# Performance work log

Measured on AMD Instinct MI355X. Metric: run time of the kernel, lower is better.

## Reference

```python
import jax, jax.numpy as jnp
import numpy as np

N_ATOMS = 25000
N_PAIRS = 500000
N_PROP = 16
C = 64          # channel width of pp/pi/ii/out layers
N_BASIS = 4     # radial basis functions per pair
DEPTH = 4       # number of GC blocks


def setup_inputs() -> dict:
    key = jax.random.key(0)
    ks = jax.random.split(key, 16)

    def w(k, shape):
        fan_in = shape[-2]
        return jax.random.normal(k, shape, jnp.float32) / jnp.sqrt(jnp.float32(fan_in))

    return {
        "ind_2": jax.random.randint(ks[0], (N_PAIRS, 2), 0, N_ATOMS),
        "prop": jax.random.normal(ks[1], (N_ATOMS, N_PROP), jnp.float32),
        "basis": jax.random.uniform(ks[2], (N_PAIRS, N_BASIS), jnp.float32),
        "pp0_w1": w(ks[3], (N_PROP, C)),
        "pp0_b1": jnp.zeros((C,), jnp.float32),
        "pp_w1": w(ks[4], (DEPTH - 1, C, C)),
        "pp_b1": jnp.zeros((DEPTH - 1, C), jnp.float32),
        "pp_w2": w(ks[5], (DEPTH, C, C)),
        "pp_b2": jnp.zeros((DEPTH, C), jnp.float32),
        "pi_w1": w(ks[6], (DEPTH, 2 * C, C)),
        "pi_b1": jnp.zeros((DEPTH, C), jnp.float32),
        "pi_w2": w(ks[7], (DEPTH, C, C * N_BASIS)),
        "pi_b2": jnp.zeros((DEPTH, C * N_BASIS), jnp.float32),
        "ii_w1": w(ks[8], (DEPTH, C, C)),
        "ii_w2": w(ks[9], (DEPTH, C, C)),
        "res0_w": w(ks[10], (N_PROP, C)),
        "out_w1": w(ks[11], (DEPTH, C, C)),
        "out_b1": jnp.zeros((DEPTH, C), jnp.float32),
        "out_w2": w(ks[12], (DEPTH, C, C)),
        "out_b2": jnp.zeros((DEPTH, C), jnp.float32),
        "out_wo": w(ks[13], (DEPTH, C, 1)),
    }


def _pinet_forward(ind_2, prop, basis,
                   pp0_w1, pp0_b1, pp_w1, pp_b1, pp_w2, pp_b2,
                   pi_w1, pi_b1, pi_w2, pi_b2,
                   ii_w1, ii_w2, res0_w,
                   out_w1, out_b1, out_w2, out_b2, out_wo):
    act = jnp.tanh
    n_atoms = prop.shape[0]
    n_basis = basis.shape[-1]
    c = pi_w2.shape[-1] // n_basis  # pi output channels
    depth = pp_w2.shape[0]
    ind_i = ind_2[:, 0]
    ind_j = ind_2[:, 1]

    p = prop
    output = jnp.zeros((n_atoms, out_wo.shape[-1]), p.dtype)
    for d in range(depth):
        # PPLayer (FFLayer with bias)
        if d == 0:
            h = act(p @ pp0_w1 + pp0_b1)
        else:
            h = act(p @ pp_w1[d - 1] + pp_b1[d - 1])
        h = act(h @ pp_w2[d] + pp_b2[d])
        # PILayer: gather pair endpoints, concat, FFLayer, basis contraction
        pij = jnp.concatenate([h[ind_i], h[ind_j]], axis=-1)  # (P, 2C)
        ww = act(pij @ pi_w1[d] + pi_b1[d])                   # (P, C)
        ww = act(ww @ pi_w2[d] + pi_b2[d])                    # (P, C*B)
        ww = ww.reshape(-1, c, n_basis)                       # (P, C, B)
        inter = jnp.einsum('pcb,pb->pc', ww, basis)           # (P, C)
        # IILayer (FFLayer, no bias)
        inter = act(inter @ ii_w1[d])
        inter = act(inter @ ii_w2[d])
        # IPLayer: scatter-sum pairs back to atoms
        newp = jax.ops.segment_sum(inter, ind_i, num_segments=n_atoms)
        # ResUpdate: linear projection if dims differ (block 0), else plain sum
        p = (p @ res0_w + newp) if d == 0 else (p + newp)
        # OutLayer: FFLayer + biasless linear, accumulated over depth
        o = act(p @ out_w1[d] + out_b1[d])
        o = act(o @ out_w2[d] + out_b2[d])
        output = output + o @ out_wo[d]
    return output


def reference(ind_2, prop, basis,
              pp0_w1, pp0_b1, pp_w1, pp_b1, pp_w2, pp_b2,
              pi_w1, pi_b1, pi_w2, pi_b2,
              ii_w1, ii_w2, res0_w,
              out_w1, out_b1, out_w2, out_b2, out_wo):
    return _pinet_forward(ind_2, prop, basis,
                          pp0_w1, pp0_b1, pp_w1, pp_b1, pp_w2, pp_b2,
                          pi_w1, pi_b1, pi_w2, pi_b2,
                          ii_w1, ii_w2, res0_w,
                          out_w1, out_b1, out_w2, out_b2, out_wo)
```

## Files before the change

kernel.cpp:

```cpp
#include <hip/hip_runtime.h>
#include <hip/hip_bf16.h>

#define N_ATOMS 25000
#define N_PAIRS 500000
#define DEPTH 4

typedef _Float16 f16x8 __attribute__((ext_vector_type(8)));
typedef float f32x16 __attribute__((ext_vector_type(16)));
typedef unsigned short u16;

__device__ __forceinline__ float tanh_fast(float x) {
    float e = __expf(2.0f * x);
    return 1.0f - 2.0f * __builtin_amdgcn_rcpf(e + 1.0f);
}

__device__ __forceinline__ void split_h(float x, u16& hi, u16& lo) {
    _Float16 h = (_Float16)x;
    _Float16 l = (_Float16)(x - (float)h);
    hi = *(u16*)&h;
    lo = *(u16*)&l;
}

__global__ __launch_bounds__(256)
void prep_kernel(const float* __restrict__ piW1, const float* __restrict__ piW2,
                 const float* __restrict__ iiW1, const float* __restrict__ iiW2,
                 u16* __restrict__ img1, u16* __restrict__ img2, u16* __restrict__ imgab) {
    int gid = blockIdx.x * 256 + threadIdx.x;
    int d = gid >> 15, e = gid & 32767;
    u16 hi, lo;
    if (e < 8192) {
        int k = e >> 6, n = e & 63;
        split_h(piW1[d * 8192 + e], hi, lo);
        int ntw = n >> 5, colb = n & 31;
        int ks = k >> 4, lh = (k >> 3) & 1, j = k & 7;
        int off = ((ntw * 8 + ks) * 64 + lh * 32 + colb) * 8 + j;
        img1[d * 16384 + 0 * 8192 + off] = hi;
        img1[d * 16384 + 1 * 8192 + off] = lo;
    } else if (e < 24576) {
        int s = e - 8192;
        int k = s >> 8, n = s & 255;
        split_h(piW2[d * 16384 + s], hi, lo);
        int ch = n >> 2, t = n & 3;
        int ntw = ch >> 5, colb = ch & 31;
        int ks = k >> 4, lh = (k >> 3) & 1, j = k & 7;
        int off = (((ntw * 4 + t) * 4 + ks) * 64 + lh * 32 + colb) * 8 + j;
        img2[d * 32768 + 0 * 16384 + off] = hi;
        img2[d * 32768 + 1 * 16384 + off] = lo;
    } else {
        int stage = (e < 28672) ? 0 : 1;
        int s = e - (stage ? 28672 : 24576);
        int k = s >> 6, n = s & 63;
        float x = stage ? iiW2[d * 4096 + s] : iiW1[d * 4096 + s];
        split_h(x, hi, lo);
        int ntw = n >> 5, colb = n & 31;
        int ks = k >> 4, lh = (k >> 3) & 1, j = k & 7;
        int off = ((ntw * 4 + ks) * 64 + lh * 32 + colb) * 8 + j;
        imgab[d * 16384 + (stage * 2 + 0) * 4096 + off] = hi;
        imgab[d * 16384 + (stage * 2 + 1) * 4096 + off] = lo;
    }
}

__global__ __launch_bounds__(256)
void prep_b2(const float* __restrict__ piB2, float* __restrict__ b2p) {
    int d = blockIdx.x, n = threadIdx.x;
    int ch = n >> 2, t = n & 3;
    int np = (ch >> 5) * 128 + t * 32 + (ch & 31);
    b2p[d * 256 + np] = piB2[d * 256 + n];
}

template <int K, bool IS_D0>
__global__ __launch_bounds__(256)
void atom_mlp(const float* __restrict__ p_in,
              const float* __restrict__ W1, const float* __restrict__ b1,
              const float* __restrict__ W2, const float* __restrict__ b2,
              const float* __restrict__ res0_w,
              _Float16* __restrict__ h_hi, _Float16* __restrict__ h_lo,
              float* __restrict__ acc_out) {
    __shared__ float sP[4][64];
    __shared__ float sH[4][64];
    int tid = threadIdx.x;
    int al = tid >> 6, c = tid & 63;
    int a = blockIdx.x * 4 + al;
    if (c < K) sP[al][c] = p_in[a * K + c];
    __syncthreads();
    float s = b1[c];
#pragma unroll
    for (int k = 0; k < K; ++k) s += sP[al][k] * W1[k * 64 + c];
    float t1 = tanh_fast(s);
    float r;
    if (IS_D0) {
        r = 0.f;
#pragma unroll
        for (int k = 0; k < 16; ++k) r += sP[al][k] * res0_w[k * 64 + c];
    } else {
        r = sP[al][c];
    }
    acc_out[a * 64 + c] = r;
    sH[al][c] = t1;
    __syncthreads();
    float s2 = b2[c];
#pragma unroll
    for (int k = 0; k < 64; ++k) s2 += sH[al][k] * W2[k * 64 + c];
    float hv = tanh_fast(s2);
    _Float16 hb = (_Float16)hv;
    h_hi[a * 64 + c] = hb;
    h_lo[a * 64 + c] = (_Float16)(hv - (float)hb);
}

__global__ __launch_bounds__(256)
void out_kernel(const float* __restrict__ p,
                const float* __restrict__ W1, const float* __restrict__ b1,
                const float* __restrict__ W2, const float* __restrict__ b2,
                const float* __restrict__ wo,
                float* __restrict__ out, int store) {
    __shared__ float sP[4][64];
    __shared__ float sH[4][64];
    int tid = threadIdx.x;
    int al = tid >> 6, c = tid & 63;
    int a = blockIdx.x * 4 + al;
    sP[al][c] = p[a * 64 + c];
    __syncthreads();
    float s = b1[c];
#pragma unroll
    for (int k = 0; k < 64; ++k) s += sP[al][k] * W1[k * 64 + c];
    sH[al][c] = tanh_fast(s);
    __syncthreads();
    float s2 = b2[c];
#pragma unroll
    for (int k = 0; k < 64; ++k) s2 += sH[al][k] * W2[k * 64 + c];
    float v = tanh_fast(s2) * wo[c];
#pragma unroll
    for (int off = 32; off > 0; off >>= 1) v += __shfl_down(v, off, 64);
    if (c == 0) {
        if (store) out[a] = v;
        else out[a] += v;
    }
}

#define MFMA __builtin_amdgcn_mfma_f32_32x32x16_f16

__global__ __launch_bounds__(512, 2)
void pair_kernel(const _Float16* __restrict__ hhi,
                 const _Float16* __restrict__ hlo,
                 const int* __restrict__ ind2,
                 const float* __restrict__ basis,
                 const u16* __restrict__ img1,
                 const u16* __restrict__ img2,
                 const u16* __restrict__ imgab,
                 const float* __restrict__ piB1,
                 const float* __restrict__ b2p,
                 float* __restrict__ accp) {
    __shared__ __attribute__((aligned(16))) _Float16 sW2[32768];
    __shared__ __attribute__((aligned(16))) _Float16 sW1lo[8192];
    __shared__ __attribute__((aligned(16))) _Float16 sA[16384];
    __shared__ __attribute__((aligned(16))) _Float16 sAlo[8192];
    __shared__ __attribute__((aligned(16))) _Float16 sPing[8192];
    __shared__ float sBas[128 * 4];
    __shared__ int sIdx[128];

    const int tid = threadIdx.x;
    for (int i = tid; i < 4096; i += 512) ((uint4*)sW2)[i] = ((const uint4*)img2)[i];
    for (int i = tid; i < 1024; i += 512) ((uint4*)sW1lo)[i] = ((const uint4*)(img1 + 8192))[i];

    const int l = tid & 63;
    const int w = tid >> 6;
    const int mt = w >> 1, ntw = w & 1;
    const int col = l & 31, kg = l >> 5;
    const int ch = ntw * 32 + col;
    const int chks = ch >> 4, chlh = (ch >> 3) & 1, chj = ch & 7;

    f16x8 w1h[8], fa[2][4], fb[2][4];
#pragma unroll
    for (int ks = 0; ks < 8; ++ks)
        w1h[ks] = *(const f16x8*)(img1 + ntw * 4096 + ks * 512 + l * 8);
#pragma unroll
    for (int hl = 0; hl < 2; ++hl)
#pragma unroll
        for (int ks = 0; ks < 4; ++ks) {
            fa[hl][ks] = *(const f16x8*)(imgab + (0 * 2 + hl) * 4096 + ntw * 2048 + ks * 512 + l * 8);
            fb[hl][ks] = *(const f16x8*)(imgab + (1 * 2 + hl) * 4096 + ntw * 2048 + ks * 512 + l * 8);
        }
    const float b1v = piB1[ch];
    float b2v[4];
#pragma unroll
    for (int t = 0; t < 4; ++t) b2v[t] = b2p[ntw * 128 + t * 32 + col];

    const int nTiles = (N_PAIRS + 127) >> 7;

    auto gather = [&](int tile) {
        int base = tile << 7;
#pragma unroll
        for (int it = 0; it < 6; ++it) {
            int id = it * 512 + tid;
            if (id < 2048) {
                int m = id >> 4, half = (id >> 3) & 1, seg = id & 7;
                int p = base + m;
                uint4 v = make_uint4(0u, 0u, 0u, 0u);
                if (p < N_PAIRS) {
                    int row = ind2[2 * p + half];
                    v = *(const uint4*)(hhi + row * 64 + seg * 8);
                }
                int mtd = m >> 5, lrow = m & 31;
                int ks = half * 4 + (seg >> 1), lh = seg & 1;
                *(uint4*)(sA + ((mtd * 8 + ks) * 64 + lh * 32 + lrow) * 8) = v;
            } else {
                int e = id - 2048;
                int m = e >> 3, seg = e & 7;
                int p = base + m;
                uint4 v = make_uint4(0u, 0u, 0u, 0u);
                if (p < N_PAIRS) {
                    int row = ind2[2 * p];
                    v = *(const uint4*)(hlo + row * 64 + seg * 8);
                }
                int mtd = m >> 5, lrow = m & 31;
                int ks = seg >> 1, lh = seg & 1;
                *(uint4*)(sAlo + ((mtd * 4 + ks) * 64 + lh * 32 + lrow) * 8) = v;
            }
        }
    };
    gather(blockIdx.x);
    __syncthreads();

    for (int tile = blockIdx.x; tile < nTiles; tile += gridDim.x) {
        const int base = tile << 7;

        if (tid < 128) {
            int p = base + tid;
            float4 bv = (p < N_PAIRS) ? ((const float4*)basis)[p] : make_float4(0.f, 0.f, 0.f, 0.f);
            *(float4*)&sBas[tid * 4] = bv;
            sIdx[tid] = (p < N_PAIRS) ? ind2[2 * p] : 0;
        }
        {
            f32x16 acc = {};
            const _Float16* ap = sA + mt * 4096 + l * 8;
            const _Float16* alop = sAlo + mt * 2048 + l * 8;
            const _Float16* blo = sW1lo + ntw * 4096 + l * 8;
#pragma unroll
            for (int ks = 0; ks < 8; ++ks) {
                f16x8 a = *(const f16x8*)(ap + ks * 512);
                acc = MFMA(a, w1h[ks], acc, 0, 0, 0);
                acc = MFMA(a, *(const f16x8*)(blo + ks * 512), acc, 0, 0, 0);
            }
#pragma unroll
            for (int ks = 0; ks < 4; ++ks) {
                f16x8 a = *(const f16x8*)(alop + ks * 512);
                acc = MFMA(a, w1h[ks], acc, 0, 0, 0);
            }
#pragma unroll
            for (int r = 0; r < 16; ++r) {
                int lrow = (r & 3) + 8 * (r >> 2) + 4 * kg;
                sPing[((mt * 4 + chks) * 64 + chlh * 32 + lrow) * 8 + chj] =
                    (_Float16)tanh_fast(acc[r] + b1v);
            }
        }
        __syncthreads();

        {
            f32x16 acc[4] = {{}, {}, {}, {}};
            const _Float16* ap = sPing + mt * 2048 + l * 8;
#pragma unroll
            for (int ks = 0; ks < 4; ++ks) {
                f16x8 a = *(const f16x8*)(ap + ks * 512);
#pragma unroll
                for (int t = 0; t < 4; ++t) {
                    acc[t] = MFMA(a, *(const f16x8*)(sW2 + ((ntw * 4 + t) * 4 + ks) * 512 + l * 8), acc[t], 0, 0, 0);
                    acc[t] = MFMA(a, *(const f16x8*)(sW2 + 16384 + ((ntw * 4 + t) * 4 + ks) * 512 + l * 8), acc[t], 0, 0, 0);
                }
            }
#pragma unroll
            for (int r = 0; r < 16; ++r) {
                int lrow = (r & 3) + 8 * (r >> 2) + 4 * kg;
                int row = mt * 32 + lrow;
                float4 bas = *(const float4*)&sBas[row * 4];
                float s = tanh_fast(acc[0][r] + b2v[0]) * bas.x
                        + tanh_fast(acc[1][r] + b2v[1]) * bas.y
                        + tanh_fast(acc[2][r] + b2v[2]) * bas.z
                        + tanh_fast(acc[3][r] + b2v[3]) * bas.w;
                sA[((mt * 4 + chks) * 64 + chlh * 32 + lrow) * 8 + chj] = (_Float16)s;
            }
        }
        __syncthreads();

        {
            f32x16 acc = {};
            const _Float16* ap = sA + mt * 2048 + l * 8;
#pragma unroll
            for (int ks = 0; ks < 4; ++ks) {
                f16x8 a = *(const f16x8*)(ap + ks * 512);
                acc = MFMA(a, fa[0][ks], acc, 0, 0, 0);
                acc = MFMA(a, fa[1][ks], acc, 0, 0, 0);
            }
#pragma unroll
            for (int r = 0; r < 16; ++r) {
                int lrow = (r & 3) + 8 * (r >> 2) + 4 * kg;
                sPing[((mt * 4 + chks) * 64 + chlh * 32 + lrow) * 8 + chj] =
                    (_Float16)tanh_fast(acc[r]);
            }
        }
        __syncthreads();

        {
            f16x8 afr[4];
            const _Float16* ap = sPing + mt * 2048 + l * 8;
#pragma unroll
            for (int ks = 0; ks < 4; ++ks) afr[ks] = *(const f16x8*)(ap + ks * 512);
            int idxr[16];
#pragma unroll
            for (int r = 0; r < 16; ++r)
                idxr[r] = sIdx[mt * 32 + (r & 3) + 8 * (r >> 2) + 4 * kg];

            gather(tile + gridDim.x);

            f32x16 acc = {};
#pragma unroll
            for (int ks = 0; ks < 4; ++ks) {
                acc = MFMA(afr[ks], fb[0][ks], acc, 0, 0, 0);
                acc = MFMA(afr[ks], fb[1][ks], acc, 0, 0, 0);
            }
#pragma unroll
            for (int r = 0; r < 16; ++r) {
                int lrow = (r & 3) + 8 * (r >> 2) + 4 * kg;
                int p = base + mt * 32 + lrow;
                if (p < N_PAIRS)
                    atomicAdd(&accp[idxr[r] * 64 + ch], tanh_fast(acc[r]));
            }
        }
        __syncthreads();
    }
}

extern "C" void kernel_launch(void* const* d_in, const int* in_sizes, int n_in,
                              void* d_out, int out_size, void* d_ws, size_t ws_size,
                              hipStream_t stream) {
    const int* ind2 = (const int*)d_in[0];
    const float* prop = (const float*)d_in[1];
    const float* basis = (const float*)d_in[2];
    const float* pp0_w1 = (const float*)d_in[3];
    const float* pp0_b1 = (const float*)d_in[4];
    const float* pp_w1 = (const float*)d_in[5];
    const float* pp_b1 = (const float*)d_in[6];
    const float* pp_w2 = (const float*)d_in[7];
    const float* pp_b2 = (const float*)d_in[8];
    const float* pi_w1 = (const float*)d_in[9];
    const float* pi_b1 = (const float*)d_in[10];
    const float* pi_w2 = (const float*)d_in[11];
    const float* pi_b2 = (const float*)d_in[12];
    const float* ii_w1 = (const float*)d_in[13];
    const float* ii_w2 = (const float*)d_in[14];
    const float* res0_w = (const float*)d_in[15];
    const float* out_w1 = (const float*)d_in[16];
    const float* out_b1 = (const float*)d_in[17];
    const float* out_w2 = (const float*)d_in[18];
    const float* out_b2 = (const float*)d_in[19];
    const float* out_wo = (const float*)d_in[20];
    float* out = (float*)d_out;

    float* B0 = (float*)d_ws;
    float* B1 = B0 + N_ATOMS * 64;
    _Float16* Hhi = (_Float16*)(B1 + N_ATOMS * 64);
    _Float16* Hlo = Hhi + N_ATOMS * 64;
    u16* img1 = (u16*)(Hlo + N_ATOMS * 64);
    u16* img2 = img1 + 4 * 16384;
    u16* imgab = img2 + 4 * 32768;
    float* b2p = (float*)(imgab + 4 * 16384);
    float* pbuf[2] = {B0, B1};

    prep_kernel<<<512, 256, 0, stream>>>(pi_w1, pi_w2, ii_w1, ii_w2, img1, img2, imgab);
    prep_b2<<<4, 256, 0, stream>>>(pi_b2, b2p);

    for (int d = 0; d < DEPTH; ++d) {
        float* acc = pbuf[d & 1];
        if (d == 0) {
            atom_mlp<16, true><<<N_ATOMS / 4, 256, 0, stream>>>(
                prop, pp0_w1, pp0_b1, pp_w2, pp_b2, res0_w, Hhi, Hlo, acc);
        } else {
            const float* pin = pbuf[(d - 1) & 1];
            atom_mlp<64, false><<<N_ATOMS / 4, 256, 0, stream>>>(
                pin, pp_w1 + (d - 1) * 4096, pp_b1 + (d - 1) * 64,
                pp_w2 + d * 4096, pp_b2 + d * 64, nullptr, Hhi, Hlo, acc);
        }
        pair_kernel<<<256, 512, 0, stream>>>(
            Hhi, Hlo, ind2, basis,
            img1 + d * 16384, img2 + d * 32768, imgab + d * 16384,
            pi_b1 + d * 64, b2p + d * 256, acc);
        out_kernel<<<N_ATOMS / 4, 256, 0, stream>>>(
            acc, out_w1 + d * 4096, out_b1 + d * 64,
            out_w2 + d * 4096, out_b2 + d * 64, out_wo + d * 64,
            out, d == 0 ? 1 : 0);
    }
}
```

Measured before the change: 1.051 ms.

## Restructure pair kernel for higher occupancy with direct global A-fragment loads

The pair kernel drops the LDS-staged gather of atom features and loads each lane's MFMA A fragments straight from global memory, keyed by per-lane prefetched index pairs. Only the high half of W2 stays in LDS; W1, the low half of W2 and the II weights are read from global/L2 inside the loop. LDS layouts gain XOR swizzles to avoid bank conflicts, and the second GEMM is split into two passes to cut accumulator registers. Launch bounds go to four blocks per CU and the grid doubles, trading the removed prefetch overlap and extra global weight traffic for more resident waves.

Result: slower. 1.459 ms (+38.9%).

```diff
diff --git a/kernel.cpp b/kernel.cpp
--- a/kernel.cpp
+++ b/kernel.cpp
@@ -139,7 +139,7 @@
 
 #define MFMA __builtin_amdgcn_mfma_f32_32x32x16_f16
 
-__global__ __launch_bounds__(512, 2)
+__global__ __launch_bounds__(512, 4)
 void pair_kernel(const _Float16* __restrict__ hhi,
                  const _Float16* __restrict__ hlo,
                  const int* __restrict__ ind2,
@@ -150,17 +150,14 @@
                  const float* __restrict__ piB1,
                  const float* __restrict__ b2p,
                  float* __restrict__ accp) {
-    __shared__ __attribute__((aligned(16))) _Float16 sW2[32768];
-    __shared__ __attribute__((aligned(16))) _Float16 sW1lo[8192];
-    __shared__ __attribute__((aligned(16))) _Float16 sA[16384];
-    __shared__ __attribute__((aligned(16))) _Float16 sAlo[8192];
+    __shared__ __attribute__((aligned(16))) _Float16 sW2hi[16384];
     __shared__ __attribute__((aligned(16))) _Float16 sPing[8192];
+    __shared__ __attribute__((aligned(16))) _Float16 sInter[8192];
     __shared__ float sBas[128 * 4];
     __shared__ int sIdx[128];
 
     const int tid = threadIdx.x;
-    for (int i = tid; i < 4096; i += 512) ((uint4*)sW2)[i] = ((const uint4*)img2)[i];
-    for (int i = tid; i < 1024; i += 512) ((uint4*)sW1lo)[i] = ((const uint4*)(img1 + 8192))[i];
+    for (int i = tid; i < 2048; i += 512) ((uint4*)sW2hi)[i] = ((const uint4*)img2)[i];
 
     const int l = tid & 63;
     const int w = tid >> 6;
@@ -168,161 +165,136 @@
     const int col = l & 31, kg = l >> 5;
     const int ch = ntw * 32 + col;
     const int chks = ch >> 4, chlh = (ch >> 3) & 1, chj = ch & 7;
-
-    f16x8 w1h[8], fa[2][4], fb[2][4];
-#pragma unroll
-    for (int ks = 0; ks < 8; ++ks)
-        w1h[ks] = *(const f16x8*)(img1 + ntw * 4096 + ks * 512 + l * 8);
-#pragma unroll
-    for (int hl = 0; hl < 2; ++hl)
-#pragma unroll
-        for (int ks = 0; ks < 4; ++ks) {
-            fa[hl][ks] = *(const f16x8*)(imgab + (0 * 2 + hl) * 4096 + ntw * 2048 + ks * 512 + l * 8);
-            fb[hl][ks] = *(const f16x8*)(imgab + (1 * 2 + hl) * 4096 + ntw * 2048 + ks * 512 + l * 8);
-        }
+    const int rr2 = (chks * 2 + chlh) ^ (kg << 2);
+    const int cbase = (mt * 4 + chks) * 512 + chlh * 256 + (rr2 << 3) + chj;
+    const int abase = kg * 256 + (((l & 31) ^ kg) << 3);
+    const int mrow = mt * 32 + col;
+
     const float b1v = piB1[ch];
     float b2v[4];
 #pragma unroll
     for (int t = 0; t < 4; ++t) b2v[t] = b2p[ntw * 128 + t * 32 + col];
 
     const int nTiles = (N_PAIRS + 127) >> 7;
-
-    auto gather = [&](int tile) {
-        int base = tile << 7;
-#pragma unroll
-        for (int it = 0; it < 6; ++it) {
-            int id = it * 512 + tid;
-            if (id < 2048) {
-                int m = id >> 4, half = (id >> 3) & 1, seg = id & 7;
-                int p = base + m;
-                uint4 v = make_uint4(0u, 0u, 0u, 0u);
-                if (p < N_PAIRS) {
-                    int row = ind2[2 * p + half];
-                    v = *(const uint4*)(hhi + row * 64 + seg * 8);
-                }
-                int mtd = m >> 5, lrow = m & 31;
-                int ks = half * 4 + (seg >> 1), lh = seg & 1;
-                *(uint4*)(sA + ((mtd * 8 + ks) * 64 + lh * 32 + lrow) * 8) = v;
-            } else {
-                int e = id - 2048;
-                int m = e >> 3, seg = e & 7;
-                int p = base + m;
-                uint4 v = make_uint4(0u, 0u, 0u, 0u);
-                if (p < N_PAIRS) {
-                    int row = ind2[2 * p];
-                    v = *(const uint4*)(hlo + row * 64 + seg * 8);
-                }
-                int mtd = m >> 5, lrow = m & 31;
-                int ks = seg >> 1, lh = seg & 1;
-                *(uint4*)(sAlo + ((mtd * 4 + ks) * 64 + lh * 32 + lrow) * 8) = v;
-            }
-        }
-    };
-    gather(blockIdx.x);
-    __syncthreads();
+    __syncthreads();
+
+    int pc0 = min(blockIdx.x * 128 + mrow, N_PAIRS - 1);
+    int2 ij = *(const int2*)(ind2 + 2 * pc0);
 
     for (int tile = blockIdx.x; tile < nTiles; tile += gridDim.x) {
         const int base = tile << 7;
 
         if (tid < 128) {
-            int p = base + tid;
-            float4 bv = (p < N_PAIRS) ? ((const float4*)basis)[p] : make_float4(0.f, 0.f, 0.f, 0.f);
-            *(float4*)&sBas[tid * 4] = bv;
-            sIdx[tid] = (p < N_PAIRS) ? ind2[2 * p] : 0;
-        }
+            int pc = min(base + tid, N_PAIRS - 1);
+            *(float4*)&sBas[tid * 4] = ((const float4*)basis)[pc];
+            sIdx[tid] = ind2[2 * pc];
+        }
+        {
+            f16x8 ai[4], aj[4], al4[4];
+            const _Float16* hri = hhi + ij.x * 64 + kg * 8;
+            const _Float16* hrj = hhi + ij.y * 64 + kg * 8;
+            const _Float16* hrl = hlo + ij.x * 64 + kg * 8;
+#pragma unroll
+            for (int ks = 0; ks < 4; ++ks) {
+                ai[ks] = *(const f16x8*)(hri + ks * 16);
+                aj[ks] = *(const f16x8*)(hrj + ks * 16);
+                al4[ks] = *(const f16x8*)(hrl + ks * 16);
+            }
+            f32x16 acc = {};
+            const u16* w1h = img1 + ntw * 4096 + l * 8;
+            const u16* w1l = img1 + 8192 + ntw * 4096 + l * 8;
+#pragma unroll
+            for (int ks = 0; ks < 4; ++ks) {
+                f16x8 whA = *(const f16x8*)(w1h + ks * 512);
+                f16x8 whB = *(const f16x8*)(w1h + (ks + 4) * 512);
+                f16x8 wlA = *(const f16x8*)(w1l + ks * 512);
+                f16x8 wlB = *(const f16x8*)(w1l + (ks + 4) * 512);
+                acc = MFMA(ai[ks], whA, acc, 0, 0, 0);
+                acc = MFMA(aj[ks], whB, acc, 0, 0, 0);
+                acc = MFMA(ai[ks], wlA, acc, 0, 0, 0);
+                acc = MFMA(aj[ks], wlB, acc, 0, 0, 0);
+                acc = MFMA(al4[ks], whA, acc, 0, 0, 0);
+            }
+#pragma unroll
+            for (int r = 0; r < 16; ++r) {
+                const int Lc = (r & 3) + 8 * (r >> 2);
+                sPing[cbase ^ (Lc << 3)] = (_Float16)tanh_fast(acc[r] + b1v);
+            }
+        }
+        __syncthreads();
+
+        {
+            float inter[16];
+#pragma unroll
+            for (int r = 0; r < 16; ++r) inter[r] = 0.f;
+#pragma unroll
+            for (int tp = 0; tp < 2; ++tp) {
+                f32x16 acc0 = {}, acc1 = {};
+                const int t0 = tp * 2, t1 = tp * 2 + 1;
+#pragma unroll
+                for (int ks = 0; ks < 4; ++ks) {
+                    f16x8 a = *(const f16x8*)(sPing + ((mt * 4 + ks) * 512 + (abase ^ (ks << 4))));
+                    const _Float16* bh0 = sW2hi + ((ntw * 4 + t0) * 4 + ks) * 512 + l * 8;
+                    const _Float16* bh1 = sW2hi + ((ntw * 4 + t1) * 4 + ks) * 512 + l * 8;
+                    const u16* bl0 = img2 + 16384 + ((ntw * 4 + t0) * 4 + ks) * 512 + l * 8;
+                    const u16* bl1 = img2 + 16384 + ((ntw * 4 + t1) * 4 + ks) * 512 + l * 8;
+                    acc0 = MFMA(a, *(const f16x8*)bh0, acc0, 0, 0, 0);
+                    acc0 = MFMA(a, *(const f16x8*)bl0, acc0, 0, 0, 0);
+                    acc1 = MFMA(a, *(const f16x8*)bh1, acc1, 0, 0, 0);
+                    acc1 = MFMA(a, *(const f16x8*)bl1, acc1, 0, 0, 0);
+                }
+#pragma unroll
+                for (int r = 0; r < 16; ++r) {
+                    const int Lc = (r & 3) + 8 * (r >> 2);
+                    const int row = mt * 32 + Lc + 4 * kg;
+                    float4 bas = *(const float4*)&sBas[row * 4];
+                    float bA = tp ? bas.z : bas.x;
+                    float bB = tp ? bas.w : bas.y;
+                    inter[r] += tanh_fast(acc0[r] + b2v[t0]) * bA
+                              + tanh_fast(acc1[r] + b2v[t1]) * bB;
+                }
+            }
+#pragma unroll
+            for (int r = 0; r < 16; ++r) {
+                const int Lc = (r & 3) + 8 * (r >> 2);
+                sInter[cbase ^ (Lc << 3)] = (_Float16)inter[r];
+            }
+        }
+        __syncthreads();
+
         {
             f32x16 acc = {};
-            const _Float16* ap = sA + mt * 4096 + l * 8;
-            const _Float16* alop = sAlo + mt * 2048 + l * 8;
-            const _Float16* blo = sW1lo + ntw * 4096 + l * 8;
-#pragma unroll
-            for (int ks = 0; ks < 8; ++ks) {
-                f16x8 a = *(const f16x8*)(ap + ks * 512);
-                acc = MFMA(a, w1h[ks], acc, 0, 0, 0);
-                acc = MFMA(a, *(const f16x8*)(blo + ks * 512), acc, 0, 0, 0);
-            }
 #pragma unroll
             for (int ks = 0; ks < 4; ++ks) {
-                f16x8 a = *(const f16x8*)(alop + ks * 512);
-                acc = MFMA(a, w1h[ks], acc, 0, 0, 0);
+                f16x8 a = *(const f16x8*)(sInter + ((mt * 4 + ks) * 512 + (abase ^ (ks << 4))));
+                f16x8 fwa = *(const f16x8*)(imgab + ntw * 2048 + ks * 512 + l * 8);
+                acc = MFMA(a, fwa, acc, 0, 0, 0);
             }
 #pragma unroll
             for (int r = 0; r < 16; ++r) {
-                int lrow = (r & 3) + 8 * (r >> 2) + 4 * kg;
-                sPing[((mt * 4 + chks) * 64 + chlh * 32 + lrow) * 8 + chj] =
-                    (_Float16)tanh_fast(acc[r] + b1v);
-            }
-        }
-        __syncthreads();
-
-        {
-            f32x16 acc[4] = {{}, {}, {}, {}};
-            const _Float16* ap = sPing + mt * 2048 + l * 8;
-#pragma unroll
-            for (int ks = 0; ks < 4; ++ks) {
-                f16x8 a = *(const f16x8*)(ap + ks * 512);
-#pragma unroll
-                for (int t = 0; t < 4; ++t) {
-                    acc[t] = MFMA(a, *(const f16x8*)(sW2 + ((ntw * 4 + t) * 4 + ks) * 512 + l * 8), acc[t], 0, 0, 0);
-                    acc[t] = MFMA(a, *(const f16x8*)(sW2 + 16384 + ((ntw * 4 + t) * 4 + ks) * 512 + l * 8), acc[t], 0, 0, 0);
-                }
-            }
-#pragma unroll
-            for (int r = 0; r < 16; ++r) {
-                int lrow = (r & 3) + 8 * (r >> 2) + 4 * kg;
-                int row = mt * 32 + lrow;
-                float4 bas = *(const float4*)&sBas[row * 4];
-                float s = tanh_fast(acc[0][r] + b2v[0]) * bas.x
-                        + tanh_fast(acc[1][r] + b2v[1]) * bas.y
-                        + tanh_fast(acc[2][r] + b2v[2]) * bas.z
-                        + tanh_fast(acc[3][r] + b2v[3]) * bas.w;
-                sA[((mt * 4 + chks) * 64 + chlh * 32 + lrow) * 8 + chj] = (_Float16)s;
+                const int Lc = (r & 3) + 8 * (r >> 2);
+                sPing[cbase ^ (Lc << 3)] = (_Float16)tanh_fast(acc[r]);
             }
         }
         __syncthreads();
 
         {
             f32x16 acc = {};
-            const _Float16* ap = sA + mt * 2048 + l * 8;
 #pragma unroll
             for (int ks = 0; ks < 4; ++ks) {
-                f16x8 a = *(const f16x8*)(ap + ks * 512);
-                acc = MFMA(a, fa[0][ks], acc, 0, 0, 0);
-                acc = MFMA(a, fa[1][ks], acc, 0, 0, 0);
-            }
+                f16x8 a = *(const f16x8*)(sPing + ((mt * 4 + ks) * 512 + (abase ^ (ks << 4))));
+                f16x8 fwb = *(const f16x8*)(imgab + 8192 + ntw * 2048 + ks * 512 + l * 8);
+                acc = MFMA(a, fwb, acc, 0, 0, 0);
+            }
+            int pcn = min((tile + gridDim.x) * 128 + mrow, N_PAIRS - 1);
+            ij = *(const int2*)(ind2 + 2 * pcn);
 #pragma unroll
             for (int r = 0; r < 16; ++r) {
-                int lrow = (r & 3) + 8 * (r >> 2) + 4 * kg;
-                sPing[((mt * 4 + chks) * 64 + chlh * 32 + lrow) * 8 + chj] =
-                    (_Float16)tanh_fast(acc[r]);
-            }
-        }
-        __syncthreads();
-
-        {
-            f16x8 afr[4];
-            const _Float16* ap = sPing + mt * 2048 + l * 8;
-#pragma unroll
-            for (int ks = 0; ks < 4; ++ks) afr[ks] = *(const f16x8*)(ap + ks * 512);
-            int idxr[16];
-#pragma unroll
-            for (int r = 0; r < 16; ++r)
-                idxr[r] = sIdx[mt * 32 + (r & 3) + 8 * (r >> 2) + 4 * kg];
-
-            gather(tile + gridDim.x);
-
-            f32x16 acc = {};
-#pragma unroll
-            for (int ks = 0; ks < 4; ++ks) {
-                acc = MFMA(afr[ks], fb[0][ks], acc, 0, 0, 0);
-                acc = MFMA(afr[ks], fb[1][ks], acc, 0, 0, 0);
-            }
-#pragma unroll
-            for (int r = 0; r < 16; ++r) {
-                int lrow = (r & 3) + 8 * (r >> 2) + 4 * kg;
-                int p = base + mt * 32 + lrow;
+                const int Lc = (r & 3) + 8 * (r >> 2);
+                const int lrow = Lc + 4 * kg;
+                const int p = base + mt * 32 + lrow;
                 if (p < N_PAIRS)
-                    atomicAdd(&accp[idxr[r] * 64 + ch], tanh_fast(acc[r]));
+                    atomicAdd(&accp[sIdx[mt * 32 + lrow] * 64 + ch], tanh_fast(acc[r]));
             }
         }
         __syncthreads();
@@ -379,7 +351,7 @@
                 pin, pp_w1 + (d - 1) * 4096, pp_b1 + (d - 1) * 64,
                 pp_w2 + d * 4096, pp_b2 + d * 64, nullptr, Hhi, Hlo, acc);
         }
-        pair_kernel<<<256, 512, 0, stream>>>(
+        pair_kernel<<<512, 512, 0, stream>>>(
             Hhi, Hlo, ind2, basis,
             img1 + d * 16384, img2 + d * 32768, imgab + d * 16384,
             pi_b1 + d * 64, b2p + d * 256, acc);
```
